# Performance work log

Measured on AMD Instinct MI355X. Metric: run time of the kernel, lower is better.

The kernel has to match this reference:

```python
import jax, jax.numpy as jnp
import numpy as np

B, S, D, H = 4, 2048, 256, 8
HD = D // H
SCALE = float(np.sqrt(HD))  # temperature = head_dim ** 0.5


def setup_inputs() -> dict:
    key = jax.random.key(0)
    ks = jax.random.split(key, 12)
    w = lambda k, shape: jax.random.normal(k, shape, dtype=jnp.float32) * 0.05
    x = jax.random.normal(ks[0], (B, S, D), dtype=jnp.float32)
    adj = jax.random.randint(ks[1], (B, S, S), 0, 2, dtype=jnp.int32)
    return {
        "x": x,
        "adj": adj,
        "w_qkv": w(ks[2], (3 * D, D)),
        "b_qkv": jnp.zeros((3 * D,), jnp.float32),
        "ln_g": jnp.ones((D,), jnp.float32),
        "ln_b": jnp.zeros((D,), jnp.float32),
        "w_fc": w(ks[3], (D, D)),
        "b_fc": jnp.zeros((D,), jnp.float32),
        "w_z": w(ks[4], (D, D)),
        "b_z": jnp.full((D,), -2.0, jnp.float32),  # init_bias fills w_z bias with -2
        "u_z": w(ks[5], (D, D)),
        "w_r": w(ks[6], (D, D)),
        "u_r": w(ks[7], (D, D)),
        "w_g": w(ks[8], (D, D)),
        "u_g": w(ks[9], (D, D)),
    }


def reference(x, adj, w_qkv, b_qkv, ln_g, ln_b, w_fc, b_fc,
              w_z, b_z, u_z, w_r, u_r, w_g, u_g):
    residual = x
    # LayerNorm (eps=1e-5, torch default)
    mu = jnp.mean(x, axis=-1, keepdims=True)
    var = jnp.var(x, axis=-1, keepdims=True)
    xn = (x - mu) / jnp.sqrt(var + 1e-5) * ln_g + ln_b
    # fused QKV projection -> (B*H, S, 3*HD), batch-major over (b, h)
    qkv = xn @ w_qkv.T + b_qkv                       # [B,S,3D]
    qkv = qkv.reshape(B, S, H, 3 * HD).transpose(0, 2, 1, 3).reshape(B * H, S, 3 * HD)
    q, k, v = jnp.split(qkv, 3, axis=-1)
    # masked scaled dot-product attention (full NxN scores, as in original)
    attn = jnp.einsum('nqd,nkd->nqk', q, k) / SCALE  # [B*H,S,S]
    adj_r = jnp.repeat(adj, H, axis=0)               # batch-major, matches attn layout
    attn = jnp.where(adj_r == 0, -jnp.inf, attn)
    attn = jax.nn.softmax(attn, axis=-1)
    out = jnp.einsum('nqk,nkd->nqd', attn, v)        # [B*H,S,HD]
    # Faithful replication of torch's view(n_head, batch, ...) applied to
    # batch-major data (an ordering quirk in the original module).
    out = out.reshape(H, B, S, HD).transpose(1, 2, 0, 3).reshape(B, S, D)
    y = jax.nn.relu(out @ w_fc.T + b_fc)
    # GRU gate: x=residual, y=attention branch
    z = jax.nn.sigmoid(y @ w_z.T + b_z + residual @ u_z.T)
    r = jax.nn.sigmoid(y @ w_r.T + residual @ u_r.T)
    h_hat = jnp.tanh(y @ w_g.T + (r * residual) @ u_g.T)
    return (1.0 - z) * residual + z * h_hat
```

## Files before the change

kernel.cpp:

```cpp
#include <hip/hip_runtime.h>
#include <hip/hip_bf16.h>
#include <math.h>

#define B_  4
#define S_  2048
#define D_  256
#define H_  8
#define HD_ 32
#define QSCALE 0.25504175929589786f

typedef short  bf16x8 __attribute__((ext_vector_type(8)));
typedef float  f32x4  __attribute__((ext_vector_type(4)));
typedef unsigned short ushort_t;
typedef unsigned int   uint_t;

__device__ __forceinline__ ushort_t f2b(float f) {
    union { float f; unsigned u; } v; v.f = f;
    unsigned r = (v.u + 0x7FFFu + ((v.u >> 16) & 1u)) >> 16;
    return (ushort_t)r;
}
__device__ __forceinline__ float b2f(ushort_t s) {
    return __uint_as_float((uint_t)s << 16);
}

__device__ __forceinline__ float wave_sum(float v) {
#pragma unroll
    for (int o = 32; o > 0; o >>= 1) v += __shfl_down(v, o, 64);
    return v;
}
__device__ __forceinline__ float block_sum256(float v, float* scr) {
    v = wave_sum(v);
    int lane = threadIdx.x & 63, wid = threadIdx.x >> 6;
    if (lane == 0) scr[wid] = v;
    __syncthreads();
    float r = scr[0] + scr[1] + scr[2] + scr[3];
    __syncthreads();
    return r;
}

#define WQ_SZ 196608
#define WS_SZ 65536
#define NB_ADJ 8192
#define NB_WC  2560
#define NB_LN  8192
__global__ __launch_bounds__(256)
void prep_kernel(const int* __restrict__ adj, uint_t* __restrict__ bits,
                 const float* __restrict__ w0, const float* __restrict__ w1,
                 const float* __restrict__ w2, const float* __restrict__ w3,
                 const float* __restrict__ w4, const float* __restrict__ w5,
                 const float* __restrict__ w6, const float* __restrict__ w7,
                 ushort_t* __restrict__ wout,
                 const float* __restrict__ x, const float* __restrict__ g,
                 const float* __restrict__ bb, ushort_t* __restrict__ xn_b) {
    __shared__ float scr[4];
    int blk = blockIdx.x, tid = threadIdx.x;
    if (blk < NB_ADJ) {
        int lane = tid & 63;
#pragma unroll
        for (int gp = 0; gp < 8; ++gp) {
            size_t i = ((size_t)blk * 8 + gp) * 256 + tid;
            unsigned long long m = __ballot(adj[i] != 0);
            size_t wbase = (((size_t)blk * 8 + gp) * 256 + (tid & ~63)) >> 5;
            if (lane == 0)  bits[wbase]     = (uint_t)m;
            if (lane == 32) bits[wbase + 1] = (uint_t)(m >> 32);
        }
    } else if (blk < NB_ADJ + NB_WC) {
        int idx = (blk - NB_ADJ) * 256 + tid;
        const float* src; int o;
        if (idx < WQ_SZ) { src = w0; o = idx; }
        else {
            int j = idx - WQ_SZ, seg = j >> 16; o = j & (WS_SZ - 1);
            src = (seg == 0) ? w1 : (seg == 1) ? w2 : (seg == 2) ? w3 :
                  (seg == 3) ? w4 : (seg == 4) ? w5 : (seg == 5) ? w6 : w7;
        }
        int j  = o & 7;
        int l  = (o >> 3) & 15;
        int qd = (o >> 7) & 3;
        int ks = (o >> 9) & 7;
        int ct = o >> 12;
        wout[idx] = f2b(src[(ct * 16 + l) * 256 + ks * 32 + qd * 8 + j]);
    } else {
        size_t base = (size_t)(blk - NB_ADJ - NB_WC) * D_;
        float v  = x[base + tid];
        float mu = block_sum256(v, scr) * (1.0f / D_);
        float d  = v - mu;
        float var = block_sum256(d * d, scr) * (1.0f / D_);
        float rstd = rsqrtf(var + 1e-5f);
        xn_b[base + tid] = f2b(d * rstd * g[tid] + bb[tid]);
    }
}

__global__ __launch_bounds__(256)
void gemm_qkv(const ushort_t* __restrict__ A, const ushort_t* __restrict__ Wf,
              const float* __restrict__ bias, ushort_t* __restrict__ outb,
              ushort_t* __restrict__ vT) {
    __shared__ ushort_t Sa[64][264];
    int tid = threadIdx.x;
    int wave = tid >> 6, lane = tid & 63, l = lane & 15, quad = lane >> 4;
    int wm = wave >> 1, wn = wave & 1;
    int m0 = blockIdx.y * 64, n0 = blockIdx.x * 64;
    {
        int row = tid >> 2, c0 = (tid & 3) * 64;
        const ushort_t* ap = A + (size_t)(m0 + row) * 256 + c0;
#pragma unroll
        for (int j = 0; j < 8; ++j)
            *(uint4*)&Sa[row][c0 + 8 * j] = ((const uint4*)ap)[j];
    }
    __syncthreads();

    bf16x8 af[2][8];
#pragma unroll
    for (int mt = 0; mt < 2; ++mt)
#pragma unroll
        for (int ks = 0; ks < 8; ++ks)
            af[mt][ks] = *(const bf16x8*)&Sa[wm * 32 + mt * 16 + l][ks * 32 + quad * 8];

    f32x4 acc[2][2];
#pragma unroll
    for (int i = 0; i < 2; ++i)
#pragma unroll
        for (int j = 0; j < 2; ++j) acc[i][j] = (f32x4){0.f, 0.f, 0.f, 0.f};

#pragma unroll
    for (int nt = 0; nt < 2; ++nt) {
        int ct = (n0 >> 4) + wn * 2 + nt;
        bf16x8 wfr[8];
#pragma unroll
        for (int ks = 0; ks < 8; ++ks)
            wfr[ks] = *(const bf16x8*)(Wf + (((size_t)ct * 8 + ks) * 64 + lane) * 8);
#pragma unroll
        for (int ks = 0; ks < 8; ++ks) {
            acc[0][nt] = __builtin_amdgcn_mfma_f32_16x16x32_bf16(af[0][ks], wfr[ks], acc[0][nt], 0, 0, 0);
            acc[1][nt] = __builtin_amdgcn_mfma_f32_16x16x32_bf16(af[1][ks], wfr[ks], acc[1][nt], 0, 0, 0);
        }
    }

    __syncthreads();
    ushort_t* So = &Sa[0][0];
#pragma unroll
    for (int nt = 0; nt < 2; ++nt) {
        int col = wn * 32 + nt * 16 + l;
        int gcol = n0 + col;
        float bv = bias[gcol];
        float qs = ((gcol % 96) < 32) ? QSCALE : 1.0f;
#pragma unroll
        for (int mt = 0; mt < 2; ++mt)
#pragma unroll
            for (int r = 0; r < 4; ++r) {
                int row = wm * 32 + mt * 16 + quad * 4 + r;
                So[row * 72 + col] = f2b((acc[mt][nt][r] + bv) * qs);
            }
    }
    __syncthreads();
    {
        int row = tid >> 2, seg = tid & 3;
        uint4 v0 = *(uint4*)&So[row * 72 + seg * 16];
        uint4 v1 = *(uint4*)&So[row * 72 + seg * 16 + 8];
        ushort_t* op = outb + (size_t)(m0 + row) * 768 + n0 + seg * 16;
        ((uint4*)op)[0] = v0;
        ((uint4*)op)[1] = v1;
    }

    int vs = n0 % 96;
    if (vs != 0) {
        int vloc = (vs == 64) ? 0 : 32;
        int h  = (n0 + vloc) / 96;
        int b  = m0 >> 11;
        int s0 = m0 & (S_ - 1);
        ushort_t* vstage = &Sa[0][0] + 8192;
        {
            int c = tid & 31, seg = tid >> 5;
            ushort_t tmp[8];
#pragma unroll
            for (int i = 0; i < 8; ++i)
                tmp[i] = So[(seg * 8 + i) * 72 + vloc + c];
            uint_t u[4];
#pragma unroll
            for (int i = 0; i < 4; ++i)
                u[i] = (uint_t)tmp[2 * i] | ((uint_t)tmp[2 * i + 1] << 16);
            *(uint4*)&vstage[c * 72 + seg * 8] = make_uint4(u[0], u[1], u[2], u[3]);
        }
        __syncthreads();
        {
            int d = tid >> 3, tseg = tid & 7;
            uint4 v = *(uint4*)&vstage[d * 72 + tseg * 8];
            *(uint4*)&vT[((size_t)(b * 8 + h) * 32 + d) * S_ + s0 + tseg * 8] = v;
        }
    }
}

__global__ __launch_bounds__(256)
void fused_gate(const ushort_t* __restrict__ attn_b, const float* __restrict__ xf,
                const ushort_t* __restrict__ wfc, const ushort_t* __restrict__ wz,
                const ushort_t* __restrict__ uz, const ushort_t* __restrict__ wr,
                const ushort_t* __restrict__ ur, const ushort_t* __restrict__ wg,
                const ushort_t* __restrict__ ug, const float* __restrict__ bfc,
                const float* __restrict__ bz, float* __restrict__ out) {
    __shared__ ushort_t Sa[16][264];
    __shared__ ushort_t Sx[16][264];
    __shared__ ushort_t Sy[16][264];
    __shared__ ushort_t St[16][264];
    int tid = threadIdx.x;
    int wave = tid >> 6, lane = tid & 63, l = lane & 15, quad = lane >> 4;
    int m0 = blockIdx.x * 16;
    int colbase = wave * 64;

    {
        int row = tid >> 4, c0 = (tid & 15) * 16;
        const ushort_t* ap = attn_b + (size_t)(m0 + row) * 256 + c0;
        uint4 a0 = ((const uint4*)ap)[0];
        uint4 a1 = ((const uint4*)ap)[1];
        *(uint4*)&Sa[row][c0] = a0;
        *(uint4*)&Sa[row][c0 + 8] = a1;
        const float4* xp = (const float4*)(xf + (size_t)(m0 + row) * 256 + c0);
        float4 f0 = xp[0], f1 = xp[1], f2_ = xp[2], f3 = xp[3];
        union { __hip_bfloat162 h[4]; uint4 u; } p0, p1;
        p0.h[0] = __float22bfloat162_rn(make_float2(f0.x, f0.y));
        p0.h[1] = __float22bfloat162_rn(make_float2(f0.z, f0.w));
        p0.h[2] = __float22bfloat162_rn(make_float2(f1.x, f1.y));
        p0.h[3] = __float22bfloat162_rn(make_float2(f1.z, f1.w));
        p1.h[0] = __float22bfloat162_rn(make_float2(f2_.x, f2_.y));
        p1.h[1] = __float22bfloat162_rn(make_float2(f2_.z, f2_.w));
        p1.h[2] = __float22bfloat162_rn(make_float2(f3.x, f3.y));
        p1.h[3] = __float22bfloat162_rn(make_float2(f3.z, f3.w));
        *(uint4*)&Sx[row][c0]     = p0.u;
        *(uint4*)&Sx[row][c0 + 8] = p1.u;
    }
    __syncthreads();

    {
        bf16x8 af[8];
#pragma unroll
        for (int ks = 0; ks < 8; ++ks)
            af[ks] = *(const bf16x8*)&Sa[l][ks * 32 + quad * 8];
        f32x4 ya[4];
#pragma unroll
        for (int nt = 0; nt < 4; ++nt) ya[nt] = (f32x4){0.f, 0.f, 0.f, 0.f};
#pragma unroll
        for (int nt = 0; nt < 4; ++nt) {
            size_t fb = ((size_t)(wave * 4 + nt) * 8) * 512 + lane * 8;
#pragma unroll
            for (int ks = 0; ks < 8; ++ks) {
                bf16x8 wfr = *(const bf16x8*)(wfc + fb + ks * 512);
                ya[nt] = __builtin_amdgcn_mfma_f32_16x16x32_bf16(af[ks], wfr, ya[nt], 0, 0, 0);
            }
        }
#pragma unroll
        for (int nt = 0; nt < 4; ++nt) {
            int col = colbase + nt * 16 + l;
            float bv = bfc[col];
#pragma unroll
            for (int r = 0; r < 4; ++r)
                Sy[quad * 4 + r][col] = f2b(fmaxf(ya[nt][r] + bv, 0.0f));
        }
    }
    __syncthreads();

    f32x4 az[4], ar[4], ag[4];
#pragma unroll
    for (int nt = 0; nt < 4; ++nt) {
        az[nt] = (f32x4){0.f, 0.f, 0.f, 0.f};
        ar[nt] = (f32x4){0.f, 0.f, 0.f, 0.f};
        ag[nt] = (f32x4){0.f, 0.f, 0.f, 0.f};
    }
#pragma unroll
    for (int nt = 0; nt < 4; ++nt) {
        size_t fb = ((size_t)(wave * 4 + nt) * 8) * 512 + lane * 8;
#pragma unroll
        for (int ks = 0; ks < 8; ++ks) {
            bf16x8 fy = *(const bf16x8*)&Sy[l][ks * 32 + quad * 8];
            bf16x8 fx = *(const bf16x8*)&Sx[l][ks * 32 + quad * 8];
            bf16x8 fz  = *(const bf16x8*)(wz + fb + ks * 512);
            bf16x8 fuz = *(const bf16x8*)(uz + fb + ks * 512);
            bf16x8 fr  = *(const bf16x8*)(wr + fb + ks * 512);
            bf16x8 fur = *(const bf16x8*)(ur + fb + ks * 512);
            bf16x8 fg  = *(const bf16x8*)(wg + fb + ks * 512);
            az[nt] = __builtin_amdgcn_mfma_f32_16x16x32_bf16(fy, fz,  az[nt], 0, 0, 0);
            az[nt] = __builtin_amdgcn_mfma_f32_16x16x32_bf16(fx, fuz, az[nt], 0, 0, 0);
            ar[nt] = __builtin_amdgcn_mfma_f32_16x16x32_bf16(fy, fr,  ar[nt], 0, 0, 0);
            ar[nt] = __builtin_amdgcn_mfma_f32_16x16x32_bf16(fx, fur, ar[nt], 0, 0, 0);
            ag[nt] = __builtin_amdgcn_mfma_f32_16x16x32_bf16(fy, fg,  ag[nt], 0, 0, 0);
        }
    }
#pragma unroll
    for (int nt = 0; nt < 4; ++nt) {
        int col = colbase + nt * 16 + l;
        float bzv = bz[col];
#pragma unroll
        for (int r = 0; r < 4; ++r) {
            int row = quad * 4 + r;
            az[nt][r] = 1.0f / (1.0f + __expf(-(az[nt][r] + bzv)));
            float rr  = 1.0f / (1.0f + __expf(-ar[nt][r]));
            St[row][col] = f2b(rr * b2f(Sx[row][col]));
        }
    }
    __syncthreads();

    f32x4 fcc[4];
#pragma unroll
    for (int nt = 0; nt < 4; ++nt) fcc[nt] = (f32x4){0.f, 0.f, 0.f, 0.f};
#pragma unroll
    for (int nt = 0; nt < 4; ++nt) {
        size_t fb = ((size_t)(wave * 4 + nt) * 8) * 512 + lane * 8;
#pragma unroll
        for (int ks = 0; ks < 8; ++ks) {
            bf16x8 ft = *(const bf16x8*)&St[l][ks * 32 + quad * 8];
            bf16x8 fu = *(const bf16x8*)(ug + fb + ks * 512);
            fcc[nt] = __builtin_amdgcn_mfma_f32_16x16x32_bf16(ft, fu, fcc[nt], 0, 0, 0);
        }
    }
#pragma unroll
    for (int nt = 0; nt < 4; ++nt) {
        int col = colbase + nt * 16 + l;
#pragma unroll
        for (int r = 0; r < 4; ++r) {
            int row = quad * 4 + r;
            float v = ag[nt][r] + fcc[nt][r];
            float e = __expf(2.0f * v);
            float h = 1.0f - 2.0f / (e + 1.0f);
            float zz = az[nt][r];
            size_t idx = (size_t)(m0 + row) * 256 + col;
            out[idx] = (1.0f - zz) * xf[idx] + zz * h;
        }
    }
}

__global__ __launch_bounds__(256)
void attn_kernel(const ushort_t* __restrict__ qkvb, const ushort_t* __restrict__ vT,
                 const uint_t* __restrict__ abits, ushort_t* __restrict__ attn_b) {
    __shared__ ushort_t Ks[64][40];
    __shared__ ushort_t Vt[32][72];
    __shared__ ushort_t Ps[64][72];
    __shared__ uint2   lut[16];

    int tid = threadIdx.x;
    int wave = tid >> 6, lane = tid & 63, l = lane & 15, quad = lane >> 4;
    int q0 = blockIdx.x * 64;
    int n  = blockIdx.y;
    int b = n >> 3, h = n & 7;
    int bp = n & 3, hp = n >> 2;

    if (tid < 16)
        lut[tid] = make_uint2(((tid & 1) ? 0xFFFFu : 0u) | ((tid & 2) ? 0xFFFF0000u : 0u),
                              ((tid & 4) ? 0xFFFFu : 0u) | ((tid & 8) ? 0xFFFF0000u : 0u));

    const ushort_t* base = qkvb + (size_t)b * S_ * 768 + h * 96;
    int myq = wave * 16 + l;
    int qsh = quad * 4;

    bf16x8 qf = *(const bf16x8*)(base + (size_t)(q0 + myq) * 768 + quad * 8);

    bf16x8 ones;
#pragma unroll
    for (int i = 0; i < 8; ++i) ones[i] = (short)0x3F80;

    f32x4 oacc[2], aones;
    oacc[0] = (f32x4){0.f, 0.f, 0.f, 0.f};
    oacc[1] = (f32x4){0.f, 0.f, 0.f, 0.f};
    aones   = (f32x4){0.f, 0.f, 0.f, 0.f};

    int skey = tid >> 2, spart = tid & 3;
    int kcol = (spart * 8) ^ (((skey >> 3) & 1) << 3);
    int vd = tid >> 3, vk = (tid & 7) * 8;
    const ushort_t* vptr = vT + ((size_t)n * 32 + vd) * S_ + vk;
    const uint_t* aptr = abits + ((size_t)b * S_ + q0 + myq) * 64;

    uint4 kv = *(const uint4*)(base + (size_t)skey * 768 + 32 + spart * 8);
    uint4 vv = *(const uint4*)(vptr);
    uint2 aw = *(const uint2*)(aptr);

    for (int k0 = 0; k0 < S_; k0 += 64) {
        __syncthreads();
        *(uint4*)&Ks[skey][kcol] = kv;
        *(uint4*)&Vt[vd][vk] = vv;
        uint_t aw0 = aw.x, aw1 = aw.y;
        if (k0 + 64 < S_) {
            kv = *(const uint4*)(base + (size_t)(k0 + 64 + skey) * 768 + 32 + spart * 8);
            vv = *(const uint4*)(vptr + k0 + 64);
            aw = *(const uint2*)(aptr + ((k0 + 64) >> 5));
        }
        __syncthreads();

#pragma unroll
        for (int t4 = 0; t4 < 4; ++t4) {
            bf16x8 kf = *(const bf16x8*)&Ks[t4 * 16 + l][(quad * 8) ^ ((l >> 3) << 3)];
            f32x4 z = (f32x4){0.f, 0.f, 0.f, 0.f};
            f32x4 sc = __builtin_amdgcn_mfma_f32_16x16x32_bf16(kf, qf, z, 0, 0, 0);
            uint_t w = (t4 & 2) ? aw1 : aw0;
            uint_t idx = (w >> ((t4 & 1) * 16 + qsh)) & 15u;
            uint2 mk = lut[idx];
            union { __hip_bfloat162 b2[2]; uint2 u2; } pk;
            pk.b2[0] = __float22bfloat162_rn(make_float2(exp2f(sc[0]), exp2f(sc[1])));
            pk.b2[1] = __float22bfloat162_rn(make_float2(exp2f(sc[2]), exp2f(sc[3])));
            pk.u2.x &= mk.x;
            pk.u2.y &= mk.y;
            *(uint2*)&Ps[myq][t4 * 16 + qsh] = pk.u2;
        }

#pragma unroll
        for (int ks = 0; ks < 2; ++ks) {
            bf16x8 pf = *(const bf16x8*)&Ps[wave * 16 + l][ks * 32 + quad * 8];
            aones = __builtin_amdgcn_mfma_f32_16x16x32_bf16(ones, pf, aones, 0, 0, 0);
#pragma unroll
            for (int mt = 0; mt < 2; ++mt) {
                bf16x8 vf = *(const bf16x8*)&Vt[mt * 16 + l][ks * 32 + quad * 8];
                oacc[mt] = __builtin_amdgcn_mfma_f32_16x16x32_bf16(vf, pf, oacc[mt], 0, 0, 0);
            }
        }
    }

    float linv = 1.0f / aones[0];

    __syncthreads();
    ushort_t* Ost = &Ks[0][0];
#pragma unroll
    for (int mt = 0; mt < 2; ++mt)
#pragma unroll
        for (int r = 0; r < 4; ++r)
            Ost[myq * 40 + mt * 16 + quad * 4 + r] = f2b(oacc[mt][r] * linv);
    __syncthreads();
    {
        int q = tid >> 2, part = tid & 3;
        uint4 v = *(uint4*)&Ost[q * 40 + part * 8];
        *(uint4*)&attn_b[((size_t)(bp * S_ + q0 + q)) * 256 + hp * 32 + part * 8] = v;
    }
}

extern "C" void kernel_launch(void* const* d_in, const int* in_sizes, int n_in,
                              void* d_out, int out_size, void* d_ws, size_t ws_size,
                              hipStream_t stream) {
    const float* x     = (const float*)d_in[0];
    const int*   adj   = (const int*)d_in[1];
    const float* w_qkv = (const float*)d_in[2];
    const float* b_qkv = (const float*)d_in[3];
    const float* ln_g  = (const float*)d_in[4];
    const float* ln_b  = (const float*)d_in[5];
    const float* w_fc  = (const float*)d_in[6];
    const float* b_fc  = (const float*)d_in[7];
    const float* w_z   = (const float*)d_in[8];
    const float* b_z   = (const float*)d_in[9];
    const float* u_z   = (const float*)d_in[10];
    const float* w_r   = (const float*)d_in[11];
    const float* u_r   = (const float*)d_in[12];
    const float* w_g   = (const float*)d_in[13];
    const float* u_g   = (const float*)d_in[14];
    float* out = (float*)d_out;

    const size_t TOK  = (size_t)B_ * S_;
    const size_t TOKD = TOK * D_;
    ushort_t* xn_b   = (ushort_t*)d_ws;
    ushort_t* qkv_b  = xn_b + TOKD;
    ushort_t* attn_b = qkv_b + TOK * 768;
    ushort_t* wb     = attn_b + TOKD;
    uint_t*   bits   = (uint_t*)(wb + WQ_SZ + 7 * WS_SZ);
    ushort_t* vTb    = (ushort_t*)(bits + (size_t)B_ * S_ * S_ / 32);

    ushort_t* wq_b  = wb;
    ushort_t* wfc_b = wb + WQ_SZ;
    ushort_t* wz_b  = wfc_b + WS_SZ;
    ushort_t* uz_b  = wz_b + WS_SZ;
    ushort_t* wr_b  = uz_b + WS_SZ;
    ushort_t* ur_b  = wr_b + WS_SZ;
    ushort_t* wg_b  = ur_b + WS_SZ;
    ushort_t* ug_b  = wg_b + WS_SZ;

    prep_kernel<<<NB_ADJ + NB_WC + NB_LN, 256, 0, stream>>>(
        adj, bits, w_qkv, w_fc, w_z, u_z, w_r, u_r, w_g, u_g, wb,
        x, ln_g, ln_b, xn_b);

    gemm_qkv<<<dim3(12, 128), 256, 0, stream>>>(xn_b, wq_b, b_qkv, qkv_b, vTb);

    attn_kernel<<<dim3(S_ / 64, B_ * H_), 256, 0, stream>>>(qkv_b, vTb, bits, attn_b);

    fused_gate<<<512, 256, 0, stream>>>(
        attn_b, x, wfc_b, wz_b, uz_b, wr_b, ur_b, wg_b, ug_b, b_fc, b_z, out);
}
```

Before: 235.4 us.

## Load K/V fragments directly into registers, drop block-wide LDS staging and barriers

The attention kernel no longer stages K and V tiles through shared memory with two __syncthreads per iteration. Each wave now loads its K and V MFMA fragments straight from global memory into registers, prefetching the next K tile. P and the output go through per-wave LDS slices, so no block barriers remain. It also replaces the LDS mask LUT with bit arithmetic, remaps block indices so concurrent blocks share K/V in cache, adds s_setprio around the PV MFMAs and sets a minimum-occupancy launch bound. The risks are redundant global and L2 traffic, since all four waves load the same K/V, plus higher register pressure.

```diff
diff --git a/kernel.cpp b/kernel.cpp
--- a/kernel.cpp
+++ b/kernel.cpp
@@ -325,24 +325,20 @@
     }
 }
 
-__global__ __launch_bounds__(256)
+__global__ __launch_bounds__(256, 4)
 void attn_kernel(const ushort_t* __restrict__ qkvb, const ushort_t* __restrict__ vT,
                  const uint_t* __restrict__ abits, ushort_t* __restrict__ attn_b) {
-    __shared__ ushort_t Ks[64][40];
-    __shared__ ushort_t Vt[32][72];
-    __shared__ ushort_t Ps[64][72];
-    __shared__ uint2   lut[16];
+    __shared__ ushort_t Ps[4][16][72];
 
     int tid = threadIdx.x;
     int wave = tid >> 6, lane = tid & 63, l = lane & 15, quad = lane >> 4;
-    int q0 = blockIdx.x * 64;
-    int n  = blockIdx.y;
+
+    int lid = blockIdx.y * 32 + blockIdx.x;
+    int L   = (lid & 7) * 128 + (lid >> 3);
+    int q0  = (L & 31) * 64;
+    int n   = L >> 5;
     int b = n >> 3, h = n & 7;
     int bp = n & 3, hp = n >> 2;
-
-    if (tid < 16)
-        lut[tid] = make_uint2(((tid & 1) ? 0xFFFFu : 0u) | ((tid & 2) ? 0xFFFF0000u : 0u),
-                              ((tid & 4) ? 0xFFFFu : 0u) | ((tid & 8) ? 0xFFFF0000u : 0u));
 
     const ushort_t* base = qkvb + (size_t)b * S_ * 768 + h * 96;
     int myq = wave * 16 + l;
@@ -359,70 +355,77 @@
     oacc[1] = (f32x4){0.f, 0.f, 0.f, 0.f};
     aones   = (f32x4){0.f, 0.f, 0.f, 0.f};
 
-    int skey = tid >> 2, spart = tid & 3;
-    int kcol = (spart * 8) ^ (((skey >> 3) & 1) << 3);
-    int vd = tid >> 3, vk = (tid & 7) * 8;
-    const ushort_t* vptr = vT + ((size_t)n * 32 + vd) * S_ + vk;
-    const uint_t* aptr = abits + ((size_t)b * S_ + q0 + myq) * 64;
-
-    uint4 kv = *(const uint4*)(base + (size_t)skey * 768 + 32 + spart * 8);
-    uint4 vv = *(const uint4*)(vptr);
-    uint2 aw = *(const uint2*)(aptr);
+    const uint_t*   aptr = abits + ((size_t)b * S_ + q0 + myq) * 64;
+    const ushort_t* kp = base + 32 + (size_t)l * 768 + quad * 8;
+    const ushort_t* vp = vT + ((size_t)n * 32 + l) * S_ + quad * 8;
+
+    uint2 aw = *(const uint2*)aptr;
+    bf16x8 kfr[4];
+#pragma unroll
+    for (int t4 = 0; t4 < 4; ++t4)
+        kfr[t4] = *(const bf16x8*)(kp + (size_t)(t4 * 16) * 768);
 
     for (int k0 = 0; k0 < S_; k0 += 64) {
-        __syncthreads();
-        *(uint4*)&Ks[skey][kcol] = kv;
-        *(uint4*)&Vt[vd][vk] = vv;
+        bool more = (k0 + 64 < S_);
+        bf16x8 vfr[2][2];
+#pragma unroll
+        for (int mt = 0; mt < 2; ++mt)
+#pragma unroll
+            for (int ks = 0; ks < 2; ++ks)
+                vfr[mt][ks] = *(const bf16x8*)(vp + (size_t)mt * 16 * S_ + k0 + ks * 32);
+        uint2 awn;
+        if (more) awn = *(const uint2*)(aptr + ((k0 + 64) >> 5));
         uint_t aw0 = aw.x, aw1 = aw.y;
-        if (k0 + 64 < S_) {
-            kv = *(const uint4*)(base + (size_t)(k0 + 64 + skey) * 768 + 32 + spart * 8);
-            vv = *(const uint4*)(vptr + k0 + 64);
-            aw = *(const uint2*)(aptr + ((k0 + 64) >> 5));
-        }
-        __syncthreads();
-
+
+        bf16x8 kfn[4];
 #pragma unroll
         for (int t4 = 0; t4 < 4; ++t4) {
-            bf16x8 kf = *(const bf16x8*)&Ks[t4 * 16 + l][(quad * 8) ^ ((l >> 3) << 3)];
             f32x4 z = (f32x4){0.f, 0.f, 0.f, 0.f};
-            f32x4 sc = __builtin_amdgcn_mfma_f32_16x16x32_bf16(kf, qf, z, 0, 0, 0);
+            f32x4 sc = __builtin_amdgcn_mfma_f32_16x16x32_bf16(kfr[t4], qf, z, 0, 0, 0);
+            if (more)
+                kfn[t4] = *(const bf16x8*)(kp + (size_t)(k0 + 64 + t4 * 16) * 768);
             uint_t w = (t4 & 2) ? aw1 : aw0;
             uint_t idx = (w >> ((t4 & 1) * 16 + qsh)) & 15u;
-            uint2 mk = lut[idx];
             union { __hip_bfloat162 b2[2]; uint2 u2; } pk;
             pk.b2[0] = __float22bfloat162_rn(make_float2(exp2f(sc[0]), exp2f(sc[1])));
             pk.b2[1] = __float22bfloat162_rn(make_float2(exp2f(sc[2]), exp2f(sc[3])));
-            pk.u2.x &= mk.x;
-            pk.u2.y &= mk.y;
-            *(uint2*)&Ps[myq][t4 * 16 + qsh] = pk.u2;
-        }
-
+            pk.u2.x &= ((idx & 1u) ? 0xFFFFu : 0u) | ((idx & 2u) ? 0xFFFF0000u : 0u);
+            pk.u2.y &= ((idx & 4u) ? 0xFFFFu : 0u) | ((idx & 8u) ? 0xFFFF0000u : 0u);
+            *(uint2*)&Ps[wave][l][t4 * 16 + qsh] = pk.u2;
+        }
+
+        __builtin_amdgcn_s_setprio(1);
 #pragma unroll
         for (int ks = 0; ks < 2; ++ks) {
-            bf16x8 pf = *(const bf16x8*)&Ps[wave * 16 + l][ks * 32 + quad * 8];
+            bf16x8 pf = *(const bf16x8*)&Ps[wave][l][ks * 32 + quad * 8];
             aones = __builtin_amdgcn_mfma_f32_16x16x32_bf16(ones, pf, aones, 0, 0, 0);
 #pragma unroll
-            for (int mt = 0; mt < 2; ++mt) {
-                bf16x8 vf = *(const bf16x8*)&Vt[mt * 16 + l][ks * 32 + quad * 8];
-                oacc[mt] = __builtin_amdgcn_mfma_f32_16x16x32_bf16(vf, pf, oacc[mt], 0, 0, 0);
-            }
+            for (int mt = 0; mt < 2; ++mt)
+                oacc[mt] = __builtin_amdgcn_mfma_f32_16x16x32_bf16(vfr[mt][ks], pf, oacc[mt], 0, 0, 0);
+        }
+        __builtin_amdgcn_s_setprio(0);
+
+        if (more) {
+#pragma unroll
+            for (int t4 = 0; t4 < 4; ++t4) kfr[t4] = kfn[t4];
+            aw = awn;
         }
     }
 
     float linv = 1.0f / aones[0];
 
-    __syncthreads();
-    ushort_t* Ost = &Ks[0][0];
-#pragma unroll
-    for (int mt = 0; mt < 2; ++mt)
-#pragma unroll
-        for (int r = 0; r < 4; ++r)
-            Ost[myq * 40 + mt * 16 + quad * 4 + r] = f2b(oacc[mt][r] * linv);
-    __syncthreads();
+    ushort_t* Ow = &Ps[wave][0][0];
+#pragma unroll
+    for (int mt = 0; mt < 2; ++mt) {
+        union { __hip_bfloat162 b2[2]; uint2 u2; } p;
+        p.b2[0] = __float22bfloat162_rn(make_float2(oacc[mt][0] * linv, oacc[mt][1] * linv));
+        p.b2[1] = __float22bfloat162_rn(make_float2(oacc[mt][2] * linv, oacc[mt][3] * linv));
+        *(uint2*)&Ow[l * 40 + mt * 16 + quad * 4] = p.u2;
+    }
     {
-        int q = tid >> 2, part = tid & 3;
-        uint4 v = *(uint4*)&Ost[q * 40 + part * 8];
-        *(uint4*)&attn_b[((size_t)(bp * S_ + q0 + q)) * 256 + hp * 32 + part * 8] = v;
+        int q = lane >> 2, part = lane & 3;
+        uint4 v = *(uint4*)&Ow[q * 40 + part * 8];
+        *(uint4*)&attn_b[((size_t)(bp * S_ + q0 + wave * 16 + q)) * 256 + hp * 32 + part * 8] = v;
     }
 }
 
```

Result: slower. 308.8 us (+31.2%).

## Double-buffer K/V tiles in attention kernel and remap block order

Applied to the files above, without the earlier changes.

Converts the K and V shared-memory tiles into double buffers, so the next tile is written while the current one is consumed, leaving one barrier per iteration instead of two. It also remaps the block index so neighbouring launched blocks cover different heads and batches, replaces the shared mask lookup table with inline bit arithmetic, and raises wave priority around the MFMA accumulation. The cost is more shared memory per block, which can lower occupancy, plus extra register pressure from prefetching two tiles ahead.

```diff
diff --git a/kernel.cpp b/kernel.cpp
--- a/kernel.cpp
+++ b/kernel.cpp
@@ -328,21 +328,19 @@
 __global__ __launch_bounds__(256)
 void attn_kernel(const ushort_t* __restrict__ qkvb, const ushort_t* __restrict__ vT,
                  const uint_t* __restrict__ abits, ushort_t* __restrict__ attn_b) {
-    __shared__ ushort_t Ks[64][40];
-    __shared__ ushort_t Vt[32][72];
+    __shared__ ushort_t Ks[2][64][40];
+    __shared__ ushort_t Vt[2][32][72];
     __shared__ ushort_t Ps[64][72];
-    __shared__ uint2   lut[16];
 
     int tid = threadIdx.x;
     int wave = tid >> 6, lane = tid & 63, l = lane & 15, quad = lane >> 4;
-    int q0 = blockIdx.x * 64;
-    int n  = blockIdx.y;
+
+    int lid = blockIdx.y * 32 + blockIdx.x;
+    int L   = (lid & 7) * 128 + (lid >> 3);
+    int q0  = (L & 31) * 64;
+    int n   = L >> 5;
     int b = n >> 3, h = n & 7;
     int bp = n & 3, hp = n >> 2;
-
-    if (tid < 16)
-        lut[tid] = make_uint2(((tid & 1) ? 0xFFFFu : 0u) | ((tid & 2) ? 0xFFFF0000u : 0u),
-                              ((tid & 4) ? 0xFFFFu : 0u) | ((tid & 8) ? 0xFFFF0000u : 0u));
 
     const ushort_t* base = qkvb + (size_t)b * S_ * 768 + h * 96;
     int myq = wave * 16 + l;
@@ -365,54 +363,67 @@
     const ushort_t* vptr = vT + ((size_t)n * 32 + vd) * S_ + vk;
     const uint_t* aptr = abits + ((size_t)b * S_ + q0 + myq) * 64;
 
-    uint4 kv = *(const uint4*)(base + (size_t)skey * 768 + 32 + spart * 8);
-    uint4 vv = *(const uint4*)(vptr);
     uint2 aw = *(const uint2*)(aptr);
+    {
+        uint4 k0v = *(const uint4*)(base + (size_t)skey * 768 + 32 + spart * 8);
+        uint4 v0v = *(const uint4*)(vptr);
+        *(uint4*)&Ks[0][skey][kcol] = k0v;
+        *(uint4*)&Vt[0][vd][vk] = v0v;
+    }
+    uint4 kv = *(const uint4*)(base + (size_t)(64 + skey) * 768 + 32 + spart * 8);
+    uint4 vv = *(const uint4*)(vptr + 64);
+    __syncthreads();
 
     for (int k0 = 0; k0 < S_; k0 += 64) {
-        __syncthreads();
-        *(uint4*)&Ks[skey][kcol] = kv;
-        *(uint4*)&Vt[vd][vk] = vv;
+        int cur = (k0 >> 6) & 1;
+        bool more = (k0 + 64 < S_);
+        uint2 awn;
+        if (more) {
+            *(uint4*)&Ks[cur ^ 1][skey][kcol] = kv;
+            *(uint4*)&Vt[cur ^ 1][vd][vk] = vv;
+            awn = *(const uint2*)(aptr + ((k0 + 64) >> 5));
+            if (k0 + 128 < S_) {
+                kv = *(const uint4*)(base + (size_t)(k0 + 128 + skey) * 768 + 32 + spart * 8);
+                vv = *(const uint4*)(vptr + k0 + 128);
+            }
+        }
         uint_t aw0 = aw.x, aw1 = aw.y;
-        if (k0 + 64 < S_) {
-            kv = *(const uint4*)(base + (size_t)(k0 + 64 + skey) * 768 + 32 + spart * 8);
-            vv = *(const uint4*)(vptr + k0 + 64);
-            aw = *(const uint2*)(aptr + ((k0 + 64) >> 5));
-        }
-        __syncthreads();
 
 #pragma unroll
         for (int t4 = 0; t4 < 4; ++t4) {
-            bf16x8 kf = *(const bf16x8*)&Ks[t4 * 16 + l][(quad * 8) ^ ((l >> 3) << 3)];
+            bf16x8 kf = *(const bf16x8*)&Ks[cur][t4 * 16 + l][(quad * 8) ^ ((l >> 3) << 3)];
             f32x4 z = (f32x4){0.f, 0.f, 0.f, 0.f};
             f32x4 sc = __builtin_amdgcn_mfma_f32_16x16x32_bf16(kf, qf, z, 0, 0, 0);
             uint_t w = (t4 & 2) ? aw1 : aw0;
             uint_t idx = (w >> ((t4 & 1) * 16 + qsh)) & 15u;
-            uint2 mk = lut[idx];
             union { __hip_bfloat162 b2[2]; uint2 u2; } pk;
             pk.b2[0] = __float22bfloat162_rn(make_float2(exp2f(sc[0]), exp2f(sc[1])));
             pk.b2[1] = __float22bfloat162_rn(make_float2(exp2f(sc[2]), exp2f(sc[3])));
-            pk.u2.x &= mk.x;
-            pk.u2.y &= mk.y;
+            pk.u2.x &= ((idx & 1u) ? 0xFFFFu : 0u) | ((idx & 2u) ? 0xFFFF0000u : 0u);
+            pk.u2.y &= ((idx & 4u) ? 0xFFFFu : 0u) | ((idx & 8u) ? 0xFFFF0000u : 0u);
             *(uint2*)&Ps[myq][t4 * 16 + qsh] = pk.u2;
         }
 
+        __builtin_amdgcn_s_setprio(1);
 #pragma unroll
         for (int ks = 0; ks < 2; ++ks) {
-            bf16x8 pf = *(const bf16x8*)&Ps[wave * 16 + l][ks * 32 + quad * 8];
+            bf16x8 pf = *(const bf16x8*)&Ps[myq][ks * 32 + quad * 8];
             aones = __builtin_amdgcn_mfma_f32_16x16x32_bf16(ones, pf, aones, 0, 0, 0);
 #pragma unroll
             for (int mt = 0; mt < 2; ++mt) {
-                bf16x8 vf = *(const bf16x8*)&Vt[mt * 16 + l][ks * 32 + quad * 8];
+                bf16x8 vf = *(const bf16x8*)&Vt[cur][mt * 16 + l][ks * 32 + quad * 8];
                 oacc[mt] = __builtin_amdgcn_mfma_f32_16x16x32_bf16(vf, pf, oacc[mt], 0, 0, 0);
             }
         }
+        __builtin_amdgcn_s_setprio(0);
+
+        if (more) aw = awn;
+        __syncthreads();
     }
 
     float linv = 1.0f / aones[0];
 
-    __syncthreads();
-    ushort_t* Ost = &Ks[0][0];
+    ushort_t* Ost = &Ks[0][0][0];
 #pragma unroll
     for (int mt = 0; mt < 2; ++mt)
 #pragma unroll
```

New measurement: 241.8 us. 2.7% more time.
